# Optimization experiments

Measured on AMD Instinct MI355X. Metric: run time of the kernel, lower is better.

The kernel has to match this reference:

```python
import jax, jax.numpy as jnp
import numpy as np

D_MODEL = 768
N_HEADS = 12
D_K = D_MODEL // N_HEADS


def setup_inputs() -> dict:
    key = jax.random.key(0)
    k_x, k_wqkv, k_bqkv, k_wo, k_bo = jax.random.split(key, 5)
    s = 1.0 / np.sqrt(D_MODEL)
    return {
        "x": jax.random.normal(k_x, (2, 4096, D_MODEL), dtype=jnp.float32),
        "w_qkv": jax.random.uniform(k_wqkv, (D_MODEL, 3 * D_MODEL), jnp.float32, -s, s),
        "b_qkv": jax.random.uniform(k_bqkv, (3 * D_MODEL,), jnp.float32, -s, s),
        "w_out": jax.random.uniform(k_wo, (D_MODEL, D_MODEL), jnp.float32, -s, s),
        "b_out": jax.random.uniform(k_bo, (D_MODEL,), jnp.float32, -s, s),
    }


def reference(x, w_qkv, b_qkv, w_out, b_out):
    B, S, E = x.shape
    qkv = x @ w_qkv + b_qkv                                  # [B,S,3E]
    qkv = qkv.reshape(B, S, 3, N_HEADS, D_K)
    qkv = jnp.transpose(qkv, (2, 0, 3, 1, 4))                # [3,B,H,S,Dk]
    q, k, v = qkv[0], qkv[1], qkv[2]
    scores = jnp.einsum("bhsd,bhtd->bhst", q, k) / jnp.sqrt(jnp.float32(D_K))
    attn = jax.nn.softmax(scores, axis=-1)                   # [B,H,S,S]
    ctx = jnp.einsum("bhst,bhtd->bhsd", attn, v)             # [B,H,S,Dk]
    ctx = jnp.transpose(ctx, (0, 2, 1, 3)).reshape(B, S, E)  # [B,S,E]
    return ctx @ w_out + b_out
```

## Files before the change

kernel.cpp:

```cpp
#include <hip/hip_runtime.h>

typedef short short8 __attribute__((ext_vector_type(8)));
typedef float f32x4 __attribute__((ext_vector_type(4)));
typedef float f32x16 __attribute__((ext_vector_type(16)));
typedef unsigned short u16;
typedef unsigned int u32;

__device__ __forceinline__ u16 f2bf(float f) {
  u32 u = __float_as_uint(f);
  u32 r = u + 0x7fffu + ((u >> 16) & 1u);
  return (u16)(r >> 16);
}

__device__ __forceinline__ u32 cvtpk(float lo, float hi) {
  u32 r;
  asm("v_cvt_pk_bf16_f32 %0, %1, %2" : "=v"(r) : "v"(lo), "v"(hi));
  return r;
}

__device__ __forceinline__ void async_copy16(u16* lds_dst, const u16* gsrc) {
  __builtin_amdgcn_global_load_lds(
      (const __attribute__((address_space(1))) u32*)gsrc,
      (__attribute__((address_space(3))) u32*)lds_dst, 16, 0, 0);
}

__global__ void cvt_f32_bf16(const float4* __restrict__ in, uint2* __restrict__ out, int n4) {
  int i = blockIdx.x * blockDim.x + threadIdx.x;
  if (i >= n4) return;
  float4 v = in[i];
  uint2 o;
  o.x = (u32)f2bf(v.x) | ((u32)f2bf(v.y) << 16);
  o.y = (u32)f2bf(v.z) | ((u32)f2bf(v.w) << 16);
  out[i] = o;
}

__global__ __launch_bounds__(256) void cvt_transpose_w(
    const float* __restrict__ W, u16* __restrict__ WT, int K, int N) {
  __shared__ float tl[32 * 33];
  int n0 = blockIdx.x * 32, k0 = blockIdx.y * 32;
  int tx = threadIdx.x & 31, ty = threadIdx.x >> 5;
#pragma unroll
  for (int j = 0; j < 4; ++j)
    tl[(ty + j * 8) * 33 + tx] = W[(size_t)(k0 + ty + j * 8) * N + n0 + tx];
  __syncthreads();
#pragma unroll
  for (int j = 0; j < 4; ++j)
    WT[(size_t)(n0 + ty + j * 8) * K + k0 + tx] = f2bf(tl[tx * 33 + ty + j * 8]);
}

#define BM 128
#define BN 128
#define BKG 64

template <int EPI>
__global__ __launch_bounds__(256, 2) void gemm_bf16(
    const u16* __restrict__ A, const u16* __restrict__ Bt,
    const float* __restrict__ bias, int M, int N, int K,
    u16* __restrict__ q_out, u16* __restrict__ k_out, u16* __restrict__ vt_out,
    float* __restrict__ c_out) {
  __shared__ u16 lA[BM * BKG];
  __shared__ u16 lB[BN * BKG];
  const int tid = threadIdx.x;
  const int lane = tid & 63;
  const int wid = tid >> 6;
  const int r = lane & 15, hi = lane >> 4;
  const int m0 = blockIdx.y * BM;
  const int n0 = blockIdx.x * BN;
  const int wm = (wid >> 1) * 64;
  const int wn = (wid & 1) * 64;

  f32x4 acc[4][4];
#pragma unroll
  for (int i = 0; i < 4; ++i)
#pragma unroll
    for (int j = 0; j < 4; ++j) acc[i][j] = f32x4{0.f, 0.f, 0.f, 0.f};

  for (int k0 = 0; k0 < K; k0 += BKG) {
#pragma unroll
    for (int j = 0; j < 4; ++j) {
      int cid = j * 256 + tid;
      int row = cid >> 3, c = cid & 7;
      async_copy16(&lA[cid * 8], &A[(size_t)(m0 + row) * K + k0 + c * 8]);
    }
#pragma unroll
    for (int j = 0; j < 4; ++j) {
      int cid = j * 256 + tid;
      int row = cid >> 3, c = cid & 7;
      async_copy16(&lB[cid * 8], &Bt[(size_t)(n0 + row) * K + k0 + c * 8]);
    }
    __syncthreads();
#pragma unroll
    for (int kk = 0; kk < 2; ++kk) {
      short8 af[4], bfr[4];
#pragma unroll
      for (int i = 0; i < 4; ++i)
        af[i] = *(const short8*)&lA[(wm + i * 16 + r) * BKG + kk * 32 + hi * 8];
#pragma unroll
      for (int i = 0; i < 4; ++i)
        bfr[i] = *(const short8*)&lB[(wn + i * 16 + r) * BKG + kk * 32 + hi * 8];
#pragma unroll
      for (int i = 0; i < 4; ++i)
#pragma unroll
        for (int j = 0; j < 4; ++j)
          acc[i][j] = __builtin_amdgcn_mfma_f32_16x16x32_bf16(af[i], bfr[j], acc[i][j], 0, 0, 0);
    }
    __syncthreads();
  }

#pragma unroll
  for (int i = 0; i < 4; ++i) {
#pragma unroll
    for (int j = 0; j < 4; ++j) {
      int gn = n0 + wn + j * 16 + r;
      float bv = bias[gn];
      float v0 = acc[i][j][0] + bv;
      float v1 = acc[i][j][1] + bv;
      float v2 = acc[i][j][2] + bv;
      float v3 = acc[i][j][3] + bv;
      int gm0 = m0 + wm + i * 16 + hi * 4;
      if (EPI == 1) {
        c_out[(size_t)(gm0 + 0) * N + gn] = v0;
        c_out[(size_t)(gm0 + 1) * N + gn] = v1;
        c_out[(size_t)(gm0 + 2) * N + gn] = v2;
        c_out[(size_t)(gm0 + 3) * N + gn] = v3;
      } else {
        int part = gn / 768;
        int rem = gn - part * 768;
        int h = rem >> 6, d = rem & 63;
        int b = gm0 >> 12, s = gm0 & 4095;
        if (part == 0) {
          size_t off = (((size_t)(b * 12 + h) * 4096) + s) * 64 + d;
          const float SC = 0.18033688011112042f;
          q_out[off] = f2bf(v0 * SC);
          q_out[off + 64] = f2bf(v1 * SC);
          q_out[off + 128] = f2bf(v2 * SC);
          q_out[off + 192] = f2bf(v3 * SC);
        } else if (part == 1) {
          size_t off = (((size_t)(b * 12 + h) * 4096) + s) * 64 + d;
          k_out[off] = f2bf(v0);
          k_out[off + 64] = f2bf(v1);
          k_out[off + 128] = f2bf(v2);
          k_out[off + 192] = f2bf(v3);
        } else {
          size_t off = (((size_t)(b * 12 + h) * 64) + d) * 4096 + s;
          uint2 pk;
          pk.x = (u32)f2bf(v0) | ((u32)f2bf(v1) << 16);
          pk.y = (u32)f2bf(v2) | ((u32)f2bf(v3) << 16);
          *(uint2*)&vt_out[off] = pk;
        }
      }
    }
  }
}

__global__ __launch_bounds__(256, 3) void attn_fwd(
    const u16* __restrict__ Qg, const u16* __restrict__ Kg,
    const u16* __restrict__ VTg, u16* __restrict__ ctxg) {
  __shared__ u16 lK[2][64 * 64];
  __shared__ u16 lV[2][64 * 64];
  const int tid = threadIdx.x;
  const int lane = tid & 63, wid = tid >> 6;
  const int q32 = lane & 31, half = lane >> 5;
  const int bh = blockIdx.y;
  const int s0 = blockIdx.x * 128;
  const int qrow = s0 + wid * 32 + q32;
  const u16* Qb = Qg + (size_t)bh * 4096 * 64;
  const u16* Kb = Kg + (size_t)bh * 4096 * 64;
  const u16* Vb = VTg + (size_t)bh * 64 * 4096;
  const int xorq = q32 & 7;

  short8 qf[4];
#pragma unroll
  for (int dc = 0; dc < 4; ++dc)
    qf[dc] = *(const short8*)&Qb[(size_t)qrow * 64 + dc * 16 + half * 8];

  int offlo[4], offhi[4];
#pragma unroll
  for (int i = 0; i < 4; ++i) {
    offlo[i] = q32 * 128 + (((i * 2 + half) ^ xorq) << 4);
    offhi[i] = offlo[i] + 32 * 128;
  }

  const int srow = tid >> 3, schk = (tid & 7) ^ ((tid >> 3) & 7);
  const u16* kp0 = Kb + srow * 64 + schk * 8;
  const u16* kp1 = kp0 + 32 * 64;
  const u16* vp0 = Vb + (size_t)srow * 4096 + schk * 8;
  const u16* vp1 = vp0 + (size_t)32 * 4096;

  const short8 ones8 = {0x3F80, 0x3F80, 0x3F80, 0x3F80,
                        0x3F80, 0x3F80, 0x3F80, 0x3F80};
  f32x16 zc;
#pragma unroll
  for (int i = 0; i < 16; ++i) zc[i] = 0.f;

  f32x16 acc0, acc1, acc_l;
#pragma unroll
  for (int i = 0; i < 16; ++i) { acc0[i] = 0.f; acc1[i] = 0.f; acc_l[i] = 0.f; }

#define STAGE(buf, t0_)                                            \
  do {                                                             \
    async_copy16(&lK[buf][tid * 8], kp0 + (t0_) * 64);             \
    async_copy16(&lK[buf][(256 + tid) * 8], kp1 + (t0_) * 64);     \
    async_copy16(&lV[buf][tid * 8], vp0 + (t0_));                  \
    async_copy16(&lV[buf][(256 + tid) * 8], vp1 + (t0_));          \
  } while (0)

#define PV_KS(KS)                                                              \
  {                                                                            \
    u32 x0 = w0[2 * (KS)], y0 = w0[2 * (KS) + 1];                              \
    u32 x1 = w1[2 * (KS)], y1 = w1[2 * (KS) + 1];                              \
    asm("v_permlane32_swap_b32 %0, %1" : "+v"(x0), "+v"(y0));                  \
    asm("v_permlane32_swap_b32 %0, %1" : "+v"(x1), "+v"(y1));                  \
    union { u32 u[4]; short8 s; } pa;                                          \
    pa.u[0] = x0; pa.u[1] = x1; pa.u[2] = y0; pa.u[3] = y1;                    \
    {                                                                          \
      short8 vf = *(const short8*)(lVc + offlo[KS]);                           \
      acc0 = __builtin_amdgcn_mfma_f32_32x32x16_bf16(pa.s, vf, acc0, 0, 0, 0); \
    }                                                                          \
    {                                                                          \
      short8 vf = *(const short8*)(lVc + offhi[KS]);                           \
      acc1 = __builtin_amdgcn_mfma_f32_32x32x16_bf16(pa.s, vf, acc1, 0, 0, 0); \
    }                                                                          \
    acc_l = __builtin_amdgcn_mfma_f32_32x32x16_bf16(pa.s, ones8, acc_l, 0, 0, 0); \
  }

#define SM_HALF(S, WOFF)                                                       \
  _Pragma("unroll") for (int g = 0; g < 4; ++g) {                              \
    float e0 = exp2f(S[4 * g + 0]), e1 = exp2f(S[4 * g + 1]);                  \
    float e2 = exp2f(S[4 * g + 2]), e3 = exp2f(S[4 * g + 3]);                  \
    w0[(WOFF) + g] = cvtpk(e0, e1);                                            \
    w1[(WOFF) + g] = cvtpk(e2, e3);                                            \
  }

#define ATTN_TILE(CUR, T0)                                                     \
  {                                                                            \
    __syncthreads();                                                           \
    if ((T0) + 64 < 4096) STAGE((CUR) ^ 1, (T0) + 64);                         \
    const char* lKc = (const char*)lK[CUR];                                    \
    const char* lVc = (const char*)lV[CUR];                                    \
    f32x16 sA, sB;                                                             \
    {                                                                          \
      short8 kA = *(const short8*)(lKc + offlo[0]);                            \
      sA = __builtin_amdgcn_mfma_f32_32x32x16_bf16(kA, qf[0], zc, 0, 0, 0);    \
    }                                                                          \
    _Pragma("unroll") for (int dc = 1; dc < 4; ++dc) {                         \
      short8 kA = *(const short8*)(lKc + offlo[dc]);                           \
      sA = __builtin_amdgcn_mfma_f32_32x32x16_bf16(kA, qf[dc], sA, 0, 0, 0);   \
    }                                                                          \
    {                                                                          \
      short8 kB = *(const short8*)(lKc + offhi[0]);                            \
      sB = __builtin_amdgcn_mfma_f32_32x32x16_bf16(kB, qf[0], zc, 0, 0, 0);    \
    }                                                                          \
    _Pragma("unroll") for (int dc = 1; dc < 4; ++dc) {                         \
      short8 kB = *(const short8*)(lKc + offhi[dc]);                           \
      sB = __builtin_amdgcn_mfma_f32_32x32x16_bf16(kB, qf[dc], sB, 0, 0, 0);   \
    }                                                                          \
    u32 w0[8], w1[8];                                                          \
    SM_HALF(sA, 0)                                 \
    PV_KS(0)                                                                   \
    PV_KS(1)                                                                   \
    SM_HALF(sB, 4)                              \
    PV_KS(2)                                                                   \
    PV_KS(3)                                                                   \
  }

  STAGE(0, 0);
  for (int t0 = 0; t0 < 4096; t0 += 128) {
    ATTN_TILE(0, t0);
    ATTN_TILE(1, t0 + 64);
  }

  int b = bh / 12, h = bh - b * 12;
#pragma unroll
  for (int reg = 0; reg < 16; ++reg) {
    int row = (reg & 3) + 8 * (reg >> 2) + 4 * half;
    float iv = 1.f / acc_l[reg];
    size_t base = ((size_t)b * 4096 + s0 + wid * 32 + row) * 768 + h * 64;
    ctxg[base + q32] = f2bf(acc0[reg] * iv);
    ctxg[base + 32 + q32] = f2bf(acc1[reg] * iv);
  }
}

extern "C" void kernel_launch(void* const* d_in, const int* in_sizes, int n_in,
                              void* d_out, int out_size, void* d_ws, size_t ws_size,
                              hipStream_t stream) {
  const float* x = (const float*)d_in[0];
  const float* w_qkv = (const float*)d_in[1];
  const float* b_qkv = (const float*)d_in[2];
  const float* w_out = (const float*)d_in[3];
  const float* b_out = (const float*)d_in[4];
  float* out = (float*)d_out;

  char* ws = (char*)d_ws;
  const size_t SZ_X = (size_t)8192 * 768 * 2;
  const size_t SZ_WQ = (size_t)2304 * 768 * 2;
  const size_t SZ_WO = (size_t)768 * 768 * 2;
  const size_t SZ_HSD = (size_t)24 * 4096 * 64 * 2;
  u16* xb = (u16*)ws;     ws += SZ_X;
  u16* wqkvT = (u16*)ws;  ws += SZ_WQ;
  u16* woutT = (u16*)ws;  ws += SZ_WO;
  u16* Qb = (u16*)ws;     ws += SZ_HSD;
  u16* Kb = (u16*)ws;     ws += SZ_HSD;
  u16* VTb = (u16*)ws;    ws += SZ_HSD;
  u16* ctxb = (u16*)ws;   ws += SZ_X;

  cvt_f32_bf16<<<dim3(6144), dim3(256), 0, stream>>>(
      (const float4*)x, (uint2*)xb, 8192 * 768 / 4);
  cvt_transpose_w<<<dim3(72, 24), dim3(256), 0, stream>>>(w_qkv, wqkvT, 768, 2304);
  cvt_transpose_w<<<dim3(24, 24), dim3(256), 0, stream>>>(w_out, woutT, 768, 768);
  gemm_bf16<0><<<dim3(18, 64), dim3(256), 0, stream>>>(
      xb, wqkvT, b_qkv, 8192, 2304, 768, Qb, Kb, VTb, (float*)nullptr);
  attn_fwd<<<dim3(32, 24), dim3(256), 0, stream>>>(Qb, Kb, VTb, ctxb);
  gemm_bf16<1><<<dim3(6, 64), dim3(256), 0, stream>>>(
      ctxb, woutT, b_out, 8192, 768, 768, (u16*)nullptr, (u16*)nullptr, (u16*)nullptr, out);
}
```

Measured before the change: 239.0 us.

## Split attention KV range across two blocks and combine partial results

The attention kernel now splits the 4096-long key/value sequence into two halves via a third grid dimension, doubling the block count. Each block writes unnormalized fp32 context partials and row sums, and a new combine kernel adds them, normalizes and converts to bf16. Launch bounds go from 3 to 4 blocks per CU to raise occupancy. The cost is about 100 MB of extra fp32 partial traffic, an extra kernel launch, and a grid that no longer fills a whole number of waves.

```diff
diff --git a/kernel.cpp b/kernel.cpp
--- a/kernel.cpp
+++ b/kernel.cpp
@@ -153,9 +153,10 @@
   }
 }
 
-__global__ __launch_bounds__(256, 3) void attn_fwd(
+__global__ __launch_bounds__(256, 4) void attn_fwd(
     const u16* __restrict__ Qg, const u16* __restrict__ Kg,
-    const u16* __restrict__ VTg, u16* __restrict__ ctxg) {
+    const u16* __restrict__ VTg, float* __restrict__ pctx,
+    float* __restrict__ pl) {
   __shared__ u16 lK[2][64 * 64];
   __shared__ u16 lV[2][64 * 64];
   const int tid = threadIdx.x;
@@ -163,6 +164,7 @@
   const int q32 = lane & 31, half = lane >> 5;
   const int bh = blockIdx.y;
   const int s0 = blockIdx.x * 128;
+  const int kvh = blockIdx.z;
   const int qrow = s0 + wid * 32 + q32;
   const u16* Qb = Qg + (size_t)bh * 4096 * 64;
   const u16* Kb = Kg + (size_t)bh * 4096 * 64;
@@ -182,9 +184,9 @@
   }
 
   const int srow = tid >> 3, schk = (tid & 7) ^ ((tid >> 3) & 7);
-  const u16* kp0 = Kb + srow * 64 + schk * 8;
+  const u16* kp0 = Kb + (size_t)(kvh * 2048 + srow) * 64 + schk * 8;
   const u16* kp1 = kp0 + 32 * 64;
-  const u16* vp0 = Vb + (size_t)srow * 4096 + schk * 8;
+  const u16* vp0 = Vb + (size_t)srow * 4096 + kvh * 2048 + schk * 8;
   const u16* vp1 = vp0 + (size_t)32 * 4096;
 
   const short8 ones8 = {0x3F80, 0x3F80, 0x3F80, 0x3F80,
@@ -235,7 +237,7 @@
 #define ATTN_TILE(CUR, T0)                                                     \
   {                                                                            \
     __syncthreads();                                                           \
-    if ((T0) + 64 < 4096) STAGE((CUR) ^ 1, (T0) + 64);                         \
+    if ((T0) + 64 < 2048) STAGE((CUR) ^ 1, (T0) + 64);                         \
     const char* lKc = (const char*)lK[CUR];                                    \
     const char* lVc = (const char*)lV[CUR];                                    \
     f32x16 sA, sB;                                                             \
@@ -265,20 +267,42 @@
   }
 
   STAGE(0, 0);
-  for (int t0 = 0; t0 < 4096; t0 += 128) {
+  for (int t0 = 0; t0 < 2048; t0 += 128) {
     ATTN_TILE(0, t0);
     ATTN_TILE(1, t0 + 64);
   }
 
   int b = bh / 12, h = bh - b * 12;
+  float* pc = pctx + (size_t)kvh * 8192 * 768;
+  float* plh = pl + (size_t)kvh * 24 * 4096;
 #pragma unroll
   for (int reg = 0; reg < 16; ++reg) {
     int row = (reg & 3) + 8 * (reg >> 2) + 4 * half;
-    float iv = 1.f / acc_l[reg];
-    size_t base = ((size_t)b * 4096 + s0 + wid * 32 + row) * 768 + h * 64;
-    ctxg[base + q32] = f2bf(acc0[reg] * iv);
-    ctxg[base + 32 + q32] = f2bf(acc1[reg] * iv);
-  }
+    int grow = s0 + wid * 32 + row;
+    size_t base = ((size_t)b * 4096 + grow) * 768 + h * 64;
+    pc[base + q32] = acc0[reg];
+    pc[base + 32 + q32] = acc1[reg];
+    if (q32 == 0) plh[(size_t)bh * 4096 + grow] = acc_l[reg];
+  }
+}
+
+__global__ __launch_bounds__(256) void combine_ctx(
+    const float4* __restrict__ p0, const float4* __restrict__ p1,
+    const float* __restrict__ l0, const float* __restrict__ l1,
+    uint2* __restrict__ outb) {
+  int t = blockIdx.x * 256 + threadIdx.x;
+  int s = t / 192;
+  int j = t - s * 192;
+  float4 a = p0[t], c = p1[t];
+  int h = (j * 4) >> 6;
+  int b = s >> 12, si = s & 4095;
+  int bh = b * 12 + h;
+  float l = l0[(size_t)bh * 4096 + si] + l1[(size_t)bh * 4096 + si];
+  float inv = 1.f / l;
+  uint2 o;
+  o.x = (u32)f2bf((a.x + c.x) * inv) | ((u32)f2bf((a.y + c.y) * inv) << 16);
+  o.y = (u32)f2bf((a.z + c.z) * inv) | ((u32)f2bf((a.w + c.w) * inv) << 16);
+  outb[t] = o;
 }
 
 extern "C" void kernel_launch(void* const* d_in, const int* in_sizes, int n_in,
@@ -296,6 +320,8 @@
   const size_t SZ_WQ = (size_t)2304 * 768 * 2;
   const size_t SZ_WO = (size_t)768 * 768 * 2;
   const size_t SZ_HSD = (size_t)24 * 4096 * 64 * 2;
+  const size_t SZ_PCTX = (size_t)8192 * 768 * 4;
+  const size_t SZ_PL = (size_t)24 * 4096 * 4;
   u16* xb = (u16*)ws;     ws += SZ_X;
   u16* wqkvT = (u16*)ws;  ws += SZ_WQ;
   u16* woutT = (u16*)ws;  ws += SZ_WO;
@@ -303,6 +329,8 @@
   u16* Kb = (u16*)ws;     ws += SZ_HSD;
   u16* VTb = (u16*)ws;    ws += SZ_HSD;
   u16* ctxb = (u16*)ws;   ws += SZ_X;
+  float* pctx = (float*)ws; ws += 2 * SZ_PCTX;
+  float* pl = (float*)ws;   ws += 2 * SZ_PL;
 
   cvt_f32_bf16<<<dim3(6144), dim3(256), 0, stream>>>(
       (const float4*)x, (uint2*)xb, 8192 * 768 / 4);
@@ -310,7 +338,10 @@
   cvt_transpose_w<<<dim3(24, 24), dim3(256), 0, stream>>>(w_out, woutT, 768, 768);
   gemm_bf16<0><<<dim3(18, 64), dim3(256), 0, stream>>>(
       xb, wqkvT, b_qkv, 8192, 2304, 768, Qb, Kb, VTb, (float*)nullptr);
-  attn_fwd<<<dim3(32, 24), dim3(256), 0, stream>>>(Qb, Kb, VTb, ctxb);
+  attn_fwd<<<dim3(32, 24, 2), dim3(256), 0, stream>>>(Qb, Kb, VTb, pctx, pl);
+  combine_ctx<<<dim3(6144), dim3(256), 0, stream>>>(
+      (const float4*)pctx, (const float4*)(pctx + 8192 * 768),
+      pl, pl + 24 * 4096, (uint2*)ctxb);
   gemm_bf16<1><<<dim3(6, 64), dim3(256), 0, stream>>>(
       ctxb, woutT, b_out, 8192, 768, 768, (u16*)nullptr, (u16*)nullptr, (u16*)nullptr, out);
 }
```

New measurement: 248.3 us. 3.9% more time.

## Replace async global-to-LDS copies with register-staged prefetch of K/V tiles

Applied to the files above, without the earlier changes.

The attention loop no longer uses direct global_load_lds copies. Each thread now loads the next K/V tile into registers one iteration ahead and writes those registers into the idle LDS buffer at the start of the following tile. The barrier moves to the end of each tile. The aim is to hide global latency with a longer prefetch distance, at the cost of extra VGPRs, explicit LDS stores and possibly lower occupancy.

```diff
diff --git a/kernel.cpp b/kernel.cpp
--- a/kernel.cpp
+++ b/kernel.cpp
@@ -187,6 +187,24 @@
   const u16* vp0 = Vb + (size_t)srow * 4096 + schk * 8;
   const u16* vp1 = vp0 + (size_t)32 * 4096;
 
+  short8 g0, g1, g2, g3;
+
+#define LOADG(T0_)                                              \
+  do {                                                          \
+    g0 = *(const short8*)(kp0 + (size_t)(T0_) * 64);            \
+    g1 = *(const short8*)(kp1 + (size_t)(T0_) * 64);            \
+    g2 = *(const short8*)(vp0 + (T0_));                         \
+    g3 = *(const short8*)(vp1 + (T0_));                         \
+  } while (0)
+
+#define WRITEL(BUF)                                             \
+  do {                                                          \
+    *(short8*)&lK[BUF][tid * 8] = g0;                           \
+    *(short8*)&lK[BUF][(256 + tid) * 8] = g1;                   \
+    *(short8*)&lV[BUF][tid * 8] = g2;                           \
+    *(short8*)&lV[BUF][(256 + tid) * 8] = g3;                   \
+  } while (0)
+
   const short8 ones8 = {0x3F80, 0x3F80, 0x3F80, 0x3F80,
                         0x3F80, 0x3F80, 0x3F80, 0x3F80};
   f32x16 zc;
@@ -196,14 +214,6 @@
   f32x16 acc0, acc1, acc_l;
 #pragma unroll
   for (int i = 0; i < 16; ++i) { acc0[i] = 0.f; acc1[i] = 0.f; acc_l[i] = 0.f; }
-
-#define STAGE(buf, t0_)                                            \
-  do {                                                             \
-    async_copy16(&lK[buf][tid * 8], kp0 + (t0_) * 64);             \
-    async_copy16(&lK[buf][(256 + tid) * 8], kp1 + (t0_) * 64);     \
-    async_copy16(&lV[buf][tid * 8], vp0 + (t0_));                  \
-    async_copy16(&lV[buf][(256 + tid) * 8], vp1 + (t0_));          \
-  } while (0)
 
 #define PV_KS(KS)                                                              \
   {                                                                            \
@@ -232,10 +242,10 @@
     w1[(WOFF) + g] = cvtpk(e2, e3);                                            \
   }
 
-#define ATTN_TILE(CUR, T0)                                                     \
+#define ATTN_TILE(CUR, WBUF, TLOAD)                                            \
   {                                                                            \
-    __syncthreads();                                                           \
-    if ((T0) + 64 < 4096) STAGE((CUR) ^ 1, (T0) + 64);                         \
+    WRITEL(WBUF);                                                              \
+    if ((TLOAD) < 4096) LOADG(TLOAD);                                          \
     const char* lKc = (const char*)lK[CUR];                                    \
     const char* lVc = (const char*)lV[CUR];                                    \
     f32x16 sA, sB;                                                             \
@@ -262,12 +272,17 @@
     SM_HALF(sB, 4)                              \
     PV_KS(2)                                                                   \
     PV_KS(3)                                                                   \
-  }
-
-  STAGE(0, 0);
+    __syncthreads();                                                           \
+  }
+
+  LOADG(0);
+  WRITEL(0);
+  LOADG(64);
+  __syncthreads();
+
   for (int t0 = 0; t0 < 4096; t0 += 128) {
-    ATTN_TILE(0, t0);
-    ATTN_TILE(1, t0 + 64);
+    ATTN_TILE(0, 1, t0 + 128);
+    ATTN_TILE(1, 0, t0 + 192);
   }
 
   int b = bh / 12, h = bh - b * 12;
```

Measured after the change: 238.7 us. About the same (-0.1%).

## Give each attention wave two query subtiles and compute row sums on VALU

Applied to the files above, without the earlier changes.

The attention kernel now runs 128-thread blocks in which each wave handles 64 query rows as two 32-row subtiles. Each K and V fragment read from LDS feeds MFMAs for both subtiles, halving LDS reads per query row, and K/V staging is spread over four copies per thread. The ones-vector MFMA that produced softmax denominators is replaced by VALU sums of the exponentials, combined across the two wave halves with shuffles at the end. In exchange, each wave holds more accumulators and registers, and there are fewer waves per block to hide latency.

```diff
diff --git a/kernel.cpp b/kernel.cpp
--- a/kernel.cpp
+++ b/kernel.cpp
@@ -153,7 +153,7 @@
   }
 }
 
-__global__ __launch_bounds__(256, 3) void attn_fwd(
+__global__ __launch_bounds__(128, 2) void attn_fwd(
     const u16* __restrict__ Qg, const u16* __restrict__ Kg,
     const u16* __restrict__ VTg, u16* __restrict__ ctxg) {
   __shared__ u16 lK[2][64 * 64];
@@ -163,16 +163,18 @@
   const int q32 = lane & 31, half = lane >> 5;
   const int bh = blockIdx.y;
   const int s0 = blockIdx.x * 128;
-  const int qrow = s0 + wid * 32 + q32;
   const u16* Qb = Qg + (size_t)bh * 4096 * 64;
   const u16* Kb = Kg + (size_t)bh * 4096 * 64;
   const u16* Vb = VTg + (size_t)bh * 64 * 4096;
   const int xorq = q32 & 7;
 
-  short8 qf[4];
-#pragma unroll
-  for (int dc = 0; dc < 4; ++dc)
-    qf[dc] = *(const short8*)&Qb[(size_t)qrow * 64 + dc * 16 + half * 8];
+  short8 qf[2][4];
+#pragma unroll
+  for (int s = 0; s < 2; ++s)
+#pragma unroll
+    for (int dc = 0; dc < 4; ++dc)
+      qf[s][dc] = *(const short8*)
+          &Qb[(size_t)(s0 + wid * 64 + s * 32 + q32) * 64 + dc * 16 + half * 8];
 
   int offlo[4], offhi[4];
 #pragma unroll
@@ -181,55 +183,62 @@
     offhi[i] = offlo[i] + 32 * 128;
   }
 
-  const int srow = tid >> 3, schk = (tid & 7) ^ ((tid >> 3) & 7);
-  const u16* kp0 = Kb + srow * 64 + schk * 8;
-  const u16* kp1 = kp0 + 32 * 64;
-  const u16* vp0 = Vb + (size_t)srow * 4096 + schk * 8;
-  const u16* vp1 = vp0 + (size_t)32 * 4096;
-
-  const short8 ones8 = {0x3F80, 0x3F80, 0x3F80, 0x3F80,
-                        0x3F80, 0x3F80, 0x3F80, 0x3F80};
+  const int srow = tid >> 3;
+  const int schk = (tid & 7) ^ (srow & 7);
+  const u16* kp = Kb + srow * 64 + schk * 8;
+  const u16* vp = Vb + (size_t)srow * 4096 + schk * 8;
+
   f32x16 zc;
 #pragma unroll
   for (int i = 0; i < 16; ++i) zc[i] = 0.f;
 
-  f32x16 acc0, acc1, acc_l;
-#pragma unroll
-  for (int i = 0; i < 16; ++i) { acc0[i] = 0.f; acc1[i] = 0.f; acc_l[i] = 0.f; }
-
-#define STAGE(buf, t0_)                                            \
-  do {                                                             \
-    async_copy16(&lK[buf][tid * 8], kp0 + (t0_) * 64);             \
-    async_copy16(&lK[buf][(256 + tid) * 8], kp1 + (t0_) * 64);     \
-    async_copy16(&lV[buf][tid * 8], vp0 + (t0_));                  \
-    async_copy16(&lV[buf][(256 + tid) * 8], vp1 + (t0_));          \
+  f32x16 a00, a10, a01, a11;
+#pragma unroll
+  for (int i = 0; i < 16; ++i) { a00[i] = 0.f; a10[i] = 0.f; a01[i] = 0.f; a11[i] = 0.f; }
+  float l0 = 0.f, l1 = 0.f;
+
+#define STAGE(buf, t0_)                                                        \
+  do {                                                                         \
+    _Pragma("unroll") for (int j = 0; j < 4; ++j)                              \
+      async_copy16(&lK[buf][(j * 128 + tid) * 8],                              \
+                   kp + (size_t)((t0_) + j * 16) * 64);                        \
+    _Pragma("unroll") for (int j = 0; j < 4; ++j)                              \
+      async_copy16(&lV[buf][(j * 128 + tid) * 8],                              \
+                   vp + (size_t)(j * 16) * 4096 + (t0_));                      \
   } while (0)
+
+#define SM_HALF(S, W0, W1, WOFF, LVAR)                                         \
+  _Pragma("unroll") for (int g = 0; g < 4; ++g) {                              \
+    float e0 = exp2f(S[4 * g + 0]), e1 = exp2f(S[4 * g + 1]);                  \
+    float e2 = exp2f(S[4 * g + 2]), e3 = exp2f(S[4 * g + 3]);                  \
+    W0[(WOFF) + g] = cvtpk(e0, e1);                                            \
+    W1[(WOFF) + g] = cvtpk(e2, e3);                                            \
+    LVAR += (e0 + e1) + (e2 + e3);                                             \
+  }
 
 #define PV_KS(KS)                                                              \
   {                                                                            \
-    u32 x0 = w0[2 * (KS)], y0 = w0[2 * (KS) + 1];                              \
-    u32 x1 = w1[2 * (KS)], y1 = w1[2 * (KS) + 1];                              \
-    asm("v_permlane32_swap_b32 %0, %1" : "+v"(x0), "+v"(y0));                  \
-    asm("v_permlane32_swap_b32 %0, %1" : "+v"(x1), "+v"(y1));                  \
-    union { u32 u[4]; short8 s; } pa;                                          \
-    pa.u[0] = x0; pa.u[1] = x1; pa.u[2] = y0; pa.u[3] = y1;                    \
+    u32 x0a = w0a[2 * (KS)], y0a = w0a[2 * (KS) + 1];                          \
+    u32 x1a = w1a[2 * (KS)], y1a = w1a[2 * (KS) + 1];                          \
+    u32 x0b = w0b[2 * (KS)], y0b = w0b[2 * (KS) + 1];                          \
+    u32 x1b = w1b[2 * (KS)], y1b = w1b[2 * (KS) + 1];                          \
+    asm("v_permlane32_swap_b32 %0, %1" : "+v"(x0a), "+v"(y0a));                \
+    asm("v_permlane32_swap_b32 %0, %1" : "+v"(x1a), "+v"(y1a));                \
+    asm("v_permlane32_swap_b32 %0, %1" : "+v"(x0b), "+v"(y0b));                \
+    asm("v_permlane32_swap_b32 %0, %1" : "+v"(x1b), "+v"(y1b));                \
+    union { u32 u[4]; short8 s; } pa, pb;                                      \
+    pa.u[0] = x0a; pa.u[1] = x1a; pa.u[2] = y0a; pa.u[3] = y1a;                \
+    pb.u[0] = x0b; pb.u[1] = x1b; pb.u[2] = y0b; pb.u[3] = y1b;                \
     {                                                                          \
       short8 vf = *(const short8*)(lVc + offlo[KS]);                           \
-      acc0 = __builtin_amdgcn_mfma_f32_32x32x16_bf16(pa.s, vf, acc0, 0, 0, 0); \
+      a00 = __builtin_amdgcn_mfma_f32_32x32x16_bf16(pa.s, vf, a00, 0, 0, 0);   \
+      a01 = __builtin_amdgcn_mfma_f32_32x32x16_bf16(pb.s, vf, a01, 0, 0, 0);   \
     }                                                                          \
     {                                                                          \
       short8 vf = *(const short8*)(lVc + offhi[KS]);                           \
-      acc1 = __builtin_amdgcn_mfma_f32_32x32x16_bf16(pa.s, vf, acc1, 0, 0, 0); \
+      a10 = __builtin_amdgcn_mfma_f32_32x32x16_bf16(pa.s, vf, a10, 0, 0, 0);   \
+      a11 = __builtin_amdgcn_mfma_f32_32x32x16_bf16(pb.s, vf, a11, 0, 0, 0);   \
     }                                                                          \
-    acc_l = __builtin_amdgcn_mfma_f32_32x32x16_bf16(pa.s, ones8, acc_l, 0, 0, 0); \
-  }
-
-#define SM_HALF(S, WOFF)                                                       \
-  _Pragma("unroll") for (int g = 0; g < 4; ++g) {                              \
-    float e0 = exp2f(S[4 * g + 0]), e1 = exp2f(S[4 * g + 1]);                  \
-    float e2 = exp2f(S[4 * g + 2]), e3 = exp2f(S[4 * g + 3]);                  \
-    w0[(WOFF) + g] = cvtpk(e0, e1);                                            \
-    w1[(WOFF) + g] = cvtpk(e2, e3);                                            \
   }
 
 #define ATTN_TILE(CUR, T0)                                                     \
@@ -238,28 +247,30 @@
     if ((T0) + 64 < 4096) STAGE((CUR) ^ 1, (T0) + 64);                         \
     const char* lKc = (const char*)lK[CUR];                                    \
     const char* lVc = (const char*)lV[CUR];                                    \
-    f32x16 sA, sB;                                                             \
+    f32x16 sA0, sB0, sA1, sB1;                                                 \
     {                                                                          \
       short8 kA = *(const short8*)(lKc + offlo[0]);                            \
-      sA = __builtin_amdgcn_mfma_f32_32x32x16_bf16(kA, qf[0], zc, 0, 0, 0);    \
+      short8 kB = *(const short8*)(lKc + offhi[0]);                            \
+      sA0 = __builtin_amdgcn_mfma_f32_32x32x16_bf16(kA, qf[0][0], zc, 0, 0, 0); \
+      sA1 = __builtin_amdgcn_mfma_f32_32x32x16_bf16(kA, qf[1][0], zc, 0, 0, 0); \
+      sB0 = __builtin_amdgcn_mfma_f32_32x32x16_bf16(kB, qf[0][0], zc, 0, 0, 0); \
+      sB1 = __builtin_amdgcn_mfma_f32_32x32x16_bf16(kB, qf[1][0], zc, 0, 0, 0); \
     }                                                                          \
     _Pragma("unroll") for (int dc = 1; dc < 4; ++dc) {                         \
       short8 kA = *(const short8*)(lKc + offlo[dc]);                           \
-      sA = __builtin_amdgcn_mfma_f32_32x32x16_bf16(kA, qf[dc], sA, 0, 0, 0);   \
+      short8 kB = *(const short8*)(lKc + offhi[dc]);                           \
+      sA0 = __builtin_amdgcn_mfma_f32_32x32x16_bf16(kA, qf[0][dc], sA0, 0, 0, 0); \
+      sA1 = __builtin_amdgcn_mfma_f32_32x32x16_bf16(kA, qf[1][dc], sA1, 0, 0, 0); \
+      sB0 = __builtin_amdgcn_mfma_f32_32x32x16_bf16(kB, qf[0][dc], sB0, 0, 0, 0); \
+      sB1 = __builtin_amdgcn_mfma_f32_32x32x16_bf16(kB, qf[1][dc], sB1, 0, 0, 0); \
     }                                                                          \
-    {                                                                          \
-      short8 kB = *(const short8*)(lKc + offhi[0]);                            \
-      sB = __builtin_amdgcn_mfma_f32_32x32x16_bf16(kB, qf[0], zc, 0, 0, 0);    \
-    }                                                                          \
-    _Pragma("unroll") for (int dc = 1; dc < 4; ++dc) {                         \
-      short8 kB = *(const short8*)(lKc + offhi[dc]);                           \
-      sB = __builtin_amdgcn_mfma_f32_32x32x16_bf16(kB, qf[dc], sB, 0, 0, 0);   \
-    }                                                                          \
-    u32 w0[8], w1[8];                                                          \
-    SM_HALF(sA, 0)                                 \
+    u32 w0a[8], w1a[8], w0b[8], w1b[8];                                        \
+    SM_HALF(sA0, w0a, w1a, 0, l0)                                              \
+    SM_HALF(sB0, w0a, w1a, 4, l0)                                              \
+    SM_HALF(sA1, w0b, w1b, 0, l1)                                              \
+    SM_HALF(sB1, w0b, w1b, 4, l1)                                              \
     PV_KS(0)                                                                   \
     PV_KS(1)                                                                   \
-    SM_HALF(sB, 4)                              \
     PV_KS(2)                                                                   \
     PV_KS(3)                                                                   \
   }
@@ -271,13 +282,23 @@
   }
 
   int b = bh / 12, h = bh - b * 12;
+  float inv0 = 1.f / (l0 + __shfl_xor(l0, 32));
+  float inv1 = 1.f / (l1 + __shfl_xor(l1, 32));
 #pragma unroll
   for (int reg = 0; reg < 16; ++reg) {
     int row = (reg & 3) + 8 * (reg >> 2) + 4 * half;
-    float iv = 1.f / acc_l[reg];
-    size_t base = ((size_t)b * 4096 + s0 + wid * 32 + row) * 768 + h * 64;
-    ctxg[base + q32] = f2bf(acc0[reg] * iv);
-    ctxg[base + 32 + q32] = f2bf(acc1[reg] * iv);
+    {
+      float iv = __shfl(inv0, row);
+      size_t base = ((size_t)b * 4096 + s0 + wid * 64 + row) * 768 + h * 64;
+      ctxg[base + q32] = f2bf(a00[reg] * iv);
+      ctxg[base + 32 + q32] = f2bf(a10[reg] * iv);
+    }
+    {
+      float iv = __shfl(inv1, row);
+      size_t base = ((size_t)b * 4096 + s0 + wid * 64 + 32 + row) * 768 + h * 64;
+      ctxg[base + q32] = f2bf(a01[reg] * iv);
+      ctxg[base + 32 + q32] = f2bf(a11[reg] * iv);
+    }
   }
 }
 
@@ -310,7 +331,7 @@
   cvt_transpose_w<<<dim3(24, 24), dim3(256), 0, stream>>>(w_out, woutT, 768, 768);
   gemm_bf16<0><<<dim3(18, 64), dim3(256), 0, stream>>>(
       xb, wqkvT, b_qkv, 8192, 2304, 768, Qb, Kb, VTb, (float*)nullptr);
-  attn_fwd<<<dim3(32, 24), dim3(256), 0, stream>>>(Qb, Kb, VTb, ctxb);
+  attn_fwd<<<dim3(32, 24), dim3(128), 0, stream>>>(Qb, Kb, VTb, ctxb);
   gemm_bf16<1><<<dim3(6, 64), dim3(256), 0, stream>>>(
       ctxb, woutT, b_out, 8192, 768, 768, (u16*)nullptr, (u16*)nullptr, (u16*)nullptr, out);
 }
```

Measured after the change: 265.2 us. 10.9% more time.
